# Kernel optimization log

Measured on AMD Instinct MI355X. Metric: run time of the kernel, lower is better.

Reference implementation:

```python
import jax, jax.numpy as jnp
import numpy as np

# ---- p4m group tables (g = 4*m + r, m in {0,1} mirror, r in {0..3} rot90) ----
def _p4m_tables():
    R = np.array([[0, -1], [1, 0]])
    F = np.array([[-1, 0], [0, 1]])
    I = np.eye(2, dtype=int)
    mats = []
    for m in (0, 1):
        for r in range(4):
            mats.append(np.linalg.matrix_power(R, r) @ (F if m else I))
    def idx(M):
        for i, A in enumerate(mats):
            if np.array_equal(A, M):
                return i
        raise ValueError('not in group')
    comp = np.array([[idx(mats[a] @ mats[b]) for b in range(8)] for a in range(8)])
    inv = np.array([idx(mats[a].T) for a in range(8)])  # orthogonal -> inv = transpose
    return comp, inv

COMP, INV = _p4m_tables()

def _transform_kernel(g, W):
    # L_g applied to filter spatial axes: mirror (last axis) then rotate r times
    m, r = g // 4, g % 4
    if m:
        W = jnp.flip(W, axis=-1)
    return jnp.rot90(W, k=r, axes=(-2, -1))

STRIDE, PADDING, DILATION = 1, 1, 1

def setup_inputs() -> dict:
    key = jax.random.key(0)
    k1, k2 = jax.random.split(key)
    B, Cin, Cout, H, W, kH, kW = 16, 64, 64, 64, 64, 3, 3
    x = jax.random.normal(k1, (B, Cin, 8, H, W), dtype=jnp.float32)
    scale = 1.0 / np.sqrt(Cin * kH * kW)
    weight_rel = jax.random.normal(k2, (Cout, Cin, 8, kH, kW), dtype=jnp.float32) * scale
    bias = jnp.zeros((Cout,), dtype=jnp.float32)
    return {'x': x, 'weight_rel': weight_rel, 'bias': bias}

def _gconv(x, weight_rel, bias):
    B, Cin, N, H, Wd = x.shape  # N == 8
    Cout, _, _, kH, kW = weight_rel.shape
    # Build the full group-equivariant filter bank once (fused form of the
    # original 64 small conv2d calls): bank[g*Cout+co, c*8+h] = L_g psi(g^{-1} h)
    banks = []
    for g in range(8):
        u = COMP[INV[g]]                # [8] relative element u = g^{-1} h, for h=0..7
        Wg = weight_rel[:, :, u]        # [Cout, Cin, 8, kH, kW]
        banks.append(_transform_kernel(g, Wg))
    bank = jnp.stack(banks, 0)          # [8, Cout, Cin, 8, kH, kW]
    bank = bank.reshape(8 * Cout, Cin * 8, kH, kW)
    x2 = x.reshape(B, Cin * 8, H, Wd)   # in-channel index = c*8 + h, matches bank
    y = jax.lax.conv_general_dilated(
        x2, bank,
        window_strides=(STRIDE, STRIDE),
        padding=[(PADDING, PADDING), (PADDING, PADDING)],
        rhs_dilation=(DILATION, DILATION),
        dimension_numbers=('NCHW', 'OIHW', 'NCHW'))
    Ho, Wo = y.shape[-2], y.shape[-1]
    y = y.reshape(B, 8, Cout, Ho, Wo).transpose(0, 2, 1, 3, 4)  # [B, Cout, 8, Ho, Wo]
    return y + bias[None, :, None, None, None]

def reference(x, weight_rel, bias):
    return _gconv(x, weight_rel, bias)
```

## Files before the change

### kernel.cpp

```cpp
#include <hip/hip_runtime.h>
#include <stdint.h>

typedef short  bf16x8 __attribute__((ext_vector_type(8)));
typedef float  f32x4  __attribute__((ext_vector_type(4)));


__device__ __forceinline__ short f2bf(float f) {
    uint32_t u = __builtin_bit_cast(uint32_t, f);
    u += 0x7FFFu + ((u >> 16) & 1u);
    return (short)(u >> 16);
}

__device__ __forceinline__ int u_index(int g, int s) {
    int r  = g & 3, m  = g >> 2;
    int r2 = s & 3, ms = s >> 2;
    if (!m) { int rr = (r2 - r) & 3; return ms ? (4 + rr) : rr; }
    else    { int rr = (r - r2) & 3; return ms ? rr : (4 + rr); }
}

__device__ __forceinline__ void gload_lds16(const void* g, void* l) {
    __builtin_amdgcn_global_load_lds(
        (const __attribute__((address_space(1))) uint32_t*)g,
        (__attribute__((address_space(3))) uint32_t*)l, 16, 0, 0);
}

#define XB_BYTES  (16LL * 66 * 66 * 512 * 2)
#define BK_BYTES  (16LL * 9 * 4 * 512 * 8 * 2)
#define WS_NEEDED (XB_BYTES + BK_BYTES)


__global__ __launch_bounds__(256) void prep_x2(const float* __restrict__ x,
                                               short* __restrict__ xb) {
    __shared__ float t[64][65];
    const int h = blockIdx.x, kc8 = blockIdx.y, b = blockIdx.z;
    const int k0 = kc8 * 64;
    const int tid = threadIdx.x;
    const int w  = tid & 63, kq = tid >> 6;
    const float* xp = x + ((size_t)(b * 512 + k0 + kq) * 4096) + h * 64 + w;
    #pragma unroll
    for (int i = 0; i < 16; ++i)
        t[kq + 4 * i][w] = xp[(size_t)(4 * i) * 4096];
    __syncthreads();
    const int w2 = tid >> 3, kk = tid & 7;
    #pragma unroll
    for (int half = 0; half < 2; ++half) {
        const int ww = w2 + 32 * half;
        bf16x8 v;
        #pragma unroll
        for (int j = 0; j < 8; ++j) v[j] = f2bf(t[kk * 8 + j][ww]);
        size_t o = (((size_t)b * 66 + h + 1) * 66 + (ww + 1)) * 512 + k0 + kk * 8;
        *reinterpret_cast<bf16x8*>(&xb[o]) = v;
    }
}

__global__ __launch_bounds__(256) void zero_border(short* __restrict__ xb) {
    int idx = blockIdx.x * 256 + threadIdx.x;
    if (idx >= 16 * 260 * 64) return;
    int kg = idx & 63;
    int rest = idx >> 6;
    int b  = rest / 260;
    int pe = rest - b * 260;
    int hh, ww;
    if      (pe < 66)  { hh = 0;            ww = pe; }
    else if (pe < 132) { hh = 65;           ww = pe - 66; }
    else if (pe < 196) { hh = pe - 132 + 1; ww = 0; }
    else               { hh = pe - 196 + 1; ww = 65; }
    size_t o = (((size_t)b * 66 + hh) * 66 + ww) * 512 + kg * 8;
    bf16x8 z = {0,0,0,0,0,0,0,0};
    *reinterpret_cast<bf16x8*>(&xb[o]) = z;
}

__global__ __launch_bounds__(256) void prep_w(const float* __restrict__ wrel,
                                              short* __restrict__ bank) {
    int tg = blockIdx.x * 256 + threadIdx.x;
    int oc = tg & 511;
    int kg = (tg >> 9) & 3;
    int kc = (tg >> 11) & 15;
    int t  = tg >> 15;
    int ki = t / 3, kj = t - ki * 3;
    int g = oc & 7, co = oc >> 3;
    int r = g & 3, m = g >> 2;
    int a0, b0;
    switch (r) {
        case 0:  a0 = ki;     b0 = kj;     break;
        case 1:  a0 = kj;     b0 = 2 - ki; break;
        case 2:  a0 = 2 - ki; b0 = 2 - kj; break;
        default: a0 = 2 - kj; b0 = ki;     break;
    }
    if (m) b0 = 2 - b0;
    int ci = kc * 4 + kg;
    const float* wp = wrel + (size_t)(co * 64 + ci) * 72 + a0 * 3 + b0;
    bf16x8 v;
    #pragma unroll
    for (int j = 0; j < 8; ++j) v[j] = f2bf(wp[u_index(g, j) * 9]);
    size_t o = ((((size_t)kc * 9 + t) * 4 + kg) * 512 + oc) * 8;
    *reinterpret_cast<bf16x8*>(&bank[o]) = v;
}

#define XS_SLOTS 39
#define XS_SH    (XS_SLOTS * 512)
#define WS_SH    (36 * 512)

#define STAGE(XS, WS, kc)                                                  \
    {                                                                      \
        _Pragma("unroll")                                                  \
        for (int q = 0; q < 9; ++q) {                                      \
            int it = wid + 4 * q;                                          \
            gload_lds16(bank + (size_t)(kc) * 147456 + woff[q],            \
                        &WS[it * 512]);                                    \
        }                                                                  \
        _Pragma("unroll")                                                  \
        for (int q = 0; q < 10; ++q) {                                     \
            int it = wid + 4 * q;                                          \
            if (it < XS_SLOTS)                                             \
                gload_lds16(xb + (size_t)xoff[q] + (kc) * 32,              \
                            &XS[it * 512]);                                \
        }                                                                  \
    }

#define COMPUTE(XS, WS)                                                    \
    {                                                                      \
        _Pragma("unroll")                                                  \
        for (int t = 0; t < 9; ++t) {                                      \
            const int ki = t / 3, kj = t - (t / 3) * 3;                    \
            bf16x8 a[4];                                                   \
            _Pragma("unroll")                                              \
            for (int mi = 0; mi < 4; ++mi)                                 \
                a[mi] = *reinterpret_cast<const bf16x8*>(                  \
                    &WS[((t * 4 + lkg) * 64 + mi * 16 + l15) * 8]);        \
            _Pragma("unroll")                                              \
            for (int nj = 0; nj < 8; ++nj) {                               \
                const int row = wid * 4 + (nj & 3) + ki;                   \
                const int col = (nj >> 2) * 16 + l15 + kj;                 \
                bf16x8 bv = *reinterpret_cast<const bf16x8*>(              \
                    &XS[(lkg * 624 + row * 34 + col) * 8]);                \
                _Pragma("unroll")                                          \
                for (int mi = 0; mi < 4; ++mi)                             \
                    acc[mi][nj] = __builtin_amdgcn_mfma_f32_16x16x32_bf16( \
                        a[mi], bv, acc[mi][nj], 0, 0, 0);                  \
            }                                                              \
        }                                                                  \
    }

__global__ __launch_bounds__(256, 1) void gconv_mfma(
    const short* __restrict__ xb, const short* __restrict__ bank,
    const float* __restrict__ bias, float* __restrict__ out)
{
    __shared__ __attribute__((aligned(16))) short xsA[XS_SH], xsB[XS_SH];
    __shared__ __attribute__((aligned(16))) short wsA[WS_SH], wsB[WS_SH];

    const int st  = blockIdx.x;
    const int ot  = blockIdx.y;
    const int b   = blockIdx.z;
    const int h0  = (st >> 1) * 16;
    const int w0  = (st & 1) * 32;
    const int oc0 = ot * 64;

    const int tid  = threadIdx.x;
    const int lane = tid & 63;
    const int wid  = tid >> 6;
    const int l15  = lane & 15;
    const int lkg  = lane >> 4;

    f32x4 acc[4][8];
    #pragma unroll
    for (int i = 0; i < 4; ++i)
        #pragma unroll
        for (int j = 0; j < 8; ++j)
            #pragma unroll
            for (int e = 0; e < 4; ++e) acc[i][j][e] = 0.f;

    const int xrow_base = (b * 66 + h0) * 66 + w0;

    int xoff[10];
    #pragma unroll
    for (int q = 0; q < 10; ++q) {
        int it = wid + 4 * q;
        if (it >= XS_SLOTS) it = XS_SLOTS - 1;
        int slot = it * 64 + lane;
        int kg = slot / 624;
        int px = slot - kg * 624;
        px = px < 612 ? px : 611;
        int r = px / 34;
        int c = px - r * 34;
        xoff[q] = (xrow_base + r * 66 + c) * 512 + kg * 8;
    }
    int woff[9];
    #pragma unroll
    for (int q = 0; q < 9; ++q) {
        int it = wid + 4 * q;
        int t  = it >> 2, kg = it & 3;
        woff[q] = ((t * 4 + kg) * 512 + oc0 + lane) * 8;
    }

    STAGE(xsA, wsA, 0);
    __syncthreads();
    for (int kc2 = 0; kc2 < 8; ++kc2) {
        STAGE(xsB, wsB, 2 * kc2 + 1);
        COMPUTE(xsA, wsA);
        __syncthreads();
        if (kc2 < 7) STAGE(xsA, wsA, 2 * kc2 + 2);
        COMPUTE(xsB, wsB);
        __syncthreads();
    }

    #pragma unroll
    for (int mi = 0; mi < 4; ++mi) {
        #pragma unroll
        for (int j = 0; j < 4; ++j) {
            const int oc_g = oc0 + mi * 16 + lkg * 4 + j;
            const float bv = bias[oc_g >> 3];
            float* op = out + ((size_t)b * 512 + oc_g) * 4096;
            #pragma unroll
            for (int nj = 0; nj < 8; ++nj) {
                const int hh = h0 + wid * 4 + (nj & 3);
                const int wwp = w0 + (nj >> 2) * 16 + l15;
                op[hh * 64 + wwp] = acc[mi][nj][j] + bv;
            }
        }
    }
}

__global__ __launch_bounds__(256) void gconv_direct(
    const float* __restrict__ x, const float* __restrict__ wrel,
    const float* __restrict__ bias, float* __restrict__ out)
{
    __shared__ float xsf[18][20];
    __shared__ float wsf[16][9];
    const int st = blockIdx.x, ct = blockIdx.y, b = blockIdx.z;
    const int h0 = (st >> 2) * 16, w0 = (st & 3) * 16, oc0 = ct * 16;
    const int tid = threadIdx.x;
    const int ch = tid & 15, blk = tid >> 4;
    const int by = (blk >> 2) * 4, bx = (blk & 3) * 4;
    const int oc = oc0 + ch, g = oc & 7, co = oc >> 3;
    const int wl_c = tid / 9, wl_k = tid - wl_c * 9;
    const int wl_i = wl_k / 3, wl_j = wl_k - wl_i * 3;
    const int wl_oc = oc0 + wl_c, wl_g = wl_oc & 7, wl_co = wl_oc >> 3;
    int a0, b0;
    { const int r = wl_g & 3, m = wl_g >> 2;
      switch (r) { case 0: a0=wl_i; b0=wl_j; break; case 1: a0=wl_j; b0=2-wl_i; break;
                   case 2: a0=2-wl_i; b0=2-wl_j; break; default: a0=2-wl_j; b0=wl_i; break; }
      if (m) b0 = 2 - b0; }
    float acc[4][4];
    #pragma unroll
    for (int i=0;i<4;++i) for (int j=0;j<4;++j) acc[i][j]=0.f;
    for (int t = 0; t < 512; ++t) {
        const int ci = t >> 3, s = t & 7;
        __syncthreads();
        const float* xp = x + (((size_t)(b * 64 + ci) * 8 + s) * 4096);
        for (int idx = tid; idx < 18 * 18; idx += 256) {
            const int rr = idx / 18, cc = idx - rr * 18;
            const int gh = h0 - 1 + rr, gw = w0 - 1 + cc;
            float v = 0.f;
            if (gh >= 0 && gh < 64 && gw >= 0 && gw < 64) v = xp[gh * 64 + gw];
            xsf[rr][cc] = v;
        }
        if (tid < 144) {
            const int u = u_index(wl_g, s);
            wsf[wl_c][wl_k] = wrel[((size_t)(wl_co*64+ci)*8+u)*9 + a0*3 + b0];
        }
        __syncthreads();
        float wr[9];
        #pragma unroll
        for (int k=0;k<9;++k) wr[k]=wsf[ch][k];
        float xv[6][6];
        #pragma unroll
        for (int i=0;i<6;++i) for (int j=0;j<6;++j) xv[i][j]=xsf[by+i][bx+j];
        #pragma unroll
        for (int py=0;py<4;++py) for (int px=0;px<4;++px)
            for (int ki=0;ki<3;++ki) for (int kj=0;kj<3;++kj)
                acc[py][px] += xv[py+ki][px+kj]*wr[ki*3+kj];
    }
    const float bv = bias[co];
    float* op = out + (((size_t)(b*64+co)*8+g)*4096);
    #pragma unroll
    for (int py=0;py<4;++py) for (int px=0;px<4;++px)
        op[(h0+by+py)*64 + (w0+bx+px)] = acc[py][px] + bv;
}

extern "C" void kernel_launch(void* const* d_in, const int* in_sizes, int n_in,
                              void* d_out, int out_size, void* d_ws, size_t ws_size,
                              hipStream_t stream) {
    const float* x    = (const float*)d_in[0];
    const float* wrel = (const float*)d_in[1];
    const float* bias = (const float*)d_in[2];
    float* out        = (float*)d_out;

    if (ws_size >= (size_t)WS_NEEDED) {
        short* xb   = (short*)d_ws;
        short* bank = (short*)((char*)d_ws + XB_BYTES);
        zero_border<<<1040, 256, 0, stream>>>(xb);
        {
            dim3 g(64, 8, 16);
            prep_x2<<<g, 256, 0, stream>>>(x, xb);
        }
        prep_w<<<1152, 256, 0, stream>>>(wrel, bank);
        dim3 grid(8, 8, 16);
        gconv_mfma<<<grid, 256, 0, stream>>>(xb, bank, bias, out);
    } else {
        dim3 grid(16, 32, 16);
        gconv_direct<<<grid, 256, 0, stream>>>(x, wrel, bias, out);
    }
}
```

Before: 327.5 us.

## Shrink MFMA tile to 16x16 pixels, pipeline weights per kernel column, reuse B fragments

The implicit-GEMM conv kernel's spatial tile shrinks from 16x32 to 16x16 pixels, doubling the grid. Weights are now staged per kernel column (kj), using a reordered bank layout and smaller double buffers. Each column's six input-row fragments are loaded once into registers and reused across the three ki taps. The much smaller LDS and accumulator footprint allows two blocks per CU for more latency hiding. The cost is more syncs per K chunk and more halo reloads per output, since the smaller tile overlaps its neighbours more.

```diff
diff --git a/kernel.cpp b/kernel.cpp
--- a/kernel.cpp
+++ b/kernel.cpp
@@ -93,47 +93,52 @@
     bf16x8 v;
     #pragma unroll
     for (int j = 0; j < 8; ++j) v[j] = f2bf(wp[u_index(g, j) * 9]);
-    size_t o = ((((size_t)kc * 9 + t) * 4 + kg) * 512 + oc) * 8;
+    size_t o = (((((size_t)kc * 3 + kj) * 3 + ki) * 4 + kg) * 512 + oc) * 8;
     *reinterpret_cast<bf16x8*>(&bank[o]) = v;
 }
 
-#define XS_SLOTS 39
-#define XS_SH    (XS_SLOTS * 512)
-#define WS_SH    (36 * 512)
-
-#define STAGE(XS, WS, kc)                                                  \
+#define XS_SH (1344 * 8)
+#define WB_SH (768 * 8)
+
+#define STAGE_X(XS, kc)                                                    \
     {                                                                      \
         _Pragma("unroll")                                                  \
-        for (int q = 0; q < 9; ++q) {                                      \
+        for (int q = 0; q < 6; ++q) {                                      \
             int it = wid + 4 * q;                                          \
-            gload_lds16(bank + (size_t)(kc) * 147456 + woff[q],            \
-                        &WS[it * 512]);                                    \
-        }                                                                  \
-        _Pragma("unroll")                                                  \
-        for (int q = 0; q < 10; ++q) {                                     \
-            int it = wid + 4 * q;                                          \
-            if (it < XS_SLOTS)                                             \
+            if (it < 21)                                                   \
                 gload_lds16(xb + (size_t)xoff[q] + (kc) * 32,              \
                             &XS[it * 512]);                                \
         }                                                                  \
     }
 
-#define COMPUTE(XS, WS)                                                    \
+#define STAGE_W(WB, kc, kj)                                                \
     {                                                                      \
         _Pragma("unroll")                                                  \
-        for (int t = 0; t < 9; ++t) {                                      \
-            const int ki = t / 3, kj = t - (t / 3) * 3;                    \
+        for (int q = 0; q < 3; ++q) {                                      \
+            int it = wid + 4 * q;                                          \
+            gload_lds16(bank + (size_t)((kc) * 3 + (kj)) * 49152           \
+                             + woff[q],                                    \
+                        &WB[it * 512]);                                    \
+        }                                                                  \
+    }
+
+#define COMPUTE_KJ(XS, WB, kj)                                             \
+    {                                                                      \
+        bf16x8 bfr[6];                                                     \
+        _Pragma("unroll")                                                  \
+        for (int rr = 0; rr < 6; ++rr)                                     \
+            bfr[rr] = *reinterpret_cast<const bf16x8*>(                    \
+                &XS[(lkg * 336 + (wid * 4 + rr) * 18 + l15 + (kj)) * 8]);  \
+        _Pragma("unroll")                                                  \
+        for (int ki = 0; ki < 3; ++ki) {                                   \
             bf16x8 a[4];                                                   \
             _Pragma("unroll")                                              \
             for (int mi = 0; mi < 4; ++mi)                                 \
                 a[mi] = *reinterpret_cast<const bf16x8*>(                  \
-                    &WS[((t * 4 + lkg) * 64 + mi * 16 + l15) * 8]);        \
+                    &WB[((ki * 4 + lkg) * 64 + mi * 16 + l15) * 8]);       \
             _Pragma("unroll")                                              \
-            for (int nj = 0; nj < 8; ++nj) {                               \
-                const int row = wid * 4 + (nj & 3) + ki;                   \
-                const int col = (nj >> 2) * 16 + l15 + kj;                 \
-                bf16x8 bv = *reinterpret_cast<const bf16x8*>(              \
-                    &XS[(lkg * 624 + row * 34 + col) * 8]);                \
+            for (int nj = 0; nj < 4; ++nj) {                               \
+                bf16x8 bv = bfr[nj + ki];                                  \
                 _Pragma("unroll")                                          \
                 for (int mi = 0; mi < 4; ++mi)                             \
                     acc[mi][nj] = __builtin_amdgcn_mfma_f32_16x16x32_bf16( \
@@ -142,18 +147,32 @@
         }                                                                  \
     }
 
-__global__ __launch_bounds__(256, 1) void gconv_mfma(
+#define CHUNK(kc, XC, XN, W0, W1)                                          \
+    {                                                                      \
+        STAGE_W(W1, kc, 1);                                                \
+        COMPUTE_KJ(XC, W0, 0);                                             \
+        __syncthreads();                                                   \
+        STAGE_W(W0, kc, 2);                                                \
+        if ((kc) < 15) STAGE_X(XN, (kc) + 1);                              \
+        COMPUTE_KJ(XC, W1, 1);                                             \
+        __syncthreads();                                                   \
+        if ((kc) < 15) STAGE_W(W1, (kc) + 1, 0);                           \
+        COMPUTE_KJ(XC, W0, 2);                                             \
+        __syncthreads();                                                   \
+    }
+
+__global__ __launch_bounds__(256, 2) void gconv_mfma(
     const short* __restrict__ xb, const short* __restrict__ bank,
     const float* __restrict__ bias, float* __restrict__ out)
 {
     __shared__ __attribute__((aligned(16))) short xsA[XS_SH], xsB[XS_SH];
-    __shared__ __attribute__((aligned(16))) short wsA[WS_SH], wsB[WS_SH];
+    __shared__ __attribute__((aligned(16))) short wbA[WB_SH], wbB[WB_SH];
 
     const int st  = blockIdx.x;
     const int ot  = blockIdx.y;
     const int b   = blockIdx.z;
-    const int h0  = (st >> 1) * 16;
-    const int w0  = (st & 1) * 32;
+    const int h0  = (st >> 2) * 16;
+    const int w0  = (st & 3) * 16;
     const int oc0 = ot * 64;
 
     const int tid  = threadIdx.x;
@@ -162,46 +181,42 @@
     const int l15  = lane & 15;
     const int lkg  = lane >> 4;
 
-    f32x4 acc[4][8];
+    f32x4 acc[4][4];
     #pragma unroll
     for (int i = 0; i < 4; ++i)
         #pragma unroll
-        for (int j = 0; j < 8; ++j)
+        for (int j = 0; j < 4; ++j)
             #pragma unroll
             for (int e = 0; e < 4; ++e) acc[i][j][e] = 0.f;
 
     const int xrow_base = (b * 66 + h0) * 66 + w0;
 
-    int xoff[10];
-    #pragma unroll
-    for (int q = 0; q < 10; ++q) {
+    int xoff[6];
+    #pragma unroll
+    for (int q = 0; q < 6; ++q) {
         int it = wid + 4 * q;
-        if (it >= XS_SLOTS) it = XS_SLOTS - 1;
+        if (it > 20) it = 20;
         int slot = it * 64 + lane;
-        int kg = slot / 624;
-        int px = slot - kg * 624;
-        px = px < 612 ? px : 611;
-        int r = px / 34;
-        int c = px - r * 34;
+        int kg = slot / 336;
+        int px = slot - kg * 336;
+        px = px < 324 ? px : 323;
+        int r = px / 18;
+        int c = px - r * 18;
         xoff[q] = (xrow_base + r * 66 + c) * 512 + kg * 8;
     }
-    int woff[9];
-    #pragma unroll
-    for (int q = 0; q < 9; ++q) {
+    int woff[3];
+    #pragma unroll
+    for (int q = 0; q < 3; ++q) {
         int it = wid + 4 * q;
-        int t  = it >> 2, kg = it & 3;
-        woff[q] = ((t * 4 + kg) * 512 + oc0 + lane) * 8;
-    }
-
-    STAGE(xsA, wsA, 0);
+        woff[q] = (it * 512 + oc0 + lane) * 8;
+    }
+
+    STAGE_X(xsA, 0);
+    STAGE_W(wbA, 0, 0);
     __syncthreads();
     for (int kc2 = 0; kc2 < 8; ++kc2) {
-        STAGE(xsB, wsB, 2 * kc2 + 1);
-        COMPUTE(xsA, wsA);
-        __syncthreads();
-        if (kc2 < 7) STAGE(xsA, wsA, 2 * kc2 + 2);
-        COMPUTE(xsB, wsB);
-        __syncthreads();
+        CHUNK(2 * kc2,     xsA, xsB, wbA, wbB);
+        CHUNK(2 * kc2 + 1, xsB, xsA, wbB, wbA);
     }
 
     #pragma unroll
@@ -212,10 +227,9 @@
             const float bv = bias[oc_g >> 3];
             float* op = out + ((size_t)b * 512 + oc_g) * 4096;
             #pragma unroll
-            for (int nj = 0; nj < 8; ++nj) {
-                const int hh = h0 + wid * 4 + (nj & 3);
-                const int wwp = w0 + (nj >> 2) * 16 + l15;
-                op[hh * 64 + wwp] = acc[mi][nj][j] + bv;
+            for (int nj = 0; nj < 4; ++nj) {
+                const int hh = h0 + wid * 4 + nj;
+                op[hh * 64 + w0 + l15] = acc[mi][nj][j] + bv;
             }
         }
     }
@@ -295,7 +309,7 @@
             prep_x2<<<g, 256, 0, stream>>>(x, xb);
         }
         prep_w<<<1152, 256, 0, stream>>>(wrel, bank);
-        dim3 grid(8, 8, 16);
+        dim3 grid(16, 8, 16);
         gconv_mfma<<<grid, 256, 0, stream>>>(xb, bank, bias, out);
     } else {
         dim3 grid(16, 32, 16);
```

Measured after the change: 301.7 us. 7.9% less time.

## Cache input fragments in registers across kernel rows and triple-buffer weights per column

Applied to the files above, without the earlier changes.

The filter bank is reordered so each kernel column (kj) forms its own contiguous weight slab. The main loop keeps a single input tile in LDS. For each kj it loads six input rows of B fragments into registers once and reuses them across the three kernel rows, instead of re-reading LDS for every tap. Weights are streamed through three small LDS buffers, with MFMA priority raised via setprio. LDS use is low enough for launch bounds to allow two blocks per CU; in exchange there are more barriers per channel chunk and more register pressure.

```diff
diff --git a/kernel.cpp b/kernel.cpp
--- a/kernel.cpp
+++ b/kernel.cpp
@@ -93,61 +93,75 @@
     bf16x8 v;
     #pragma unroll
     for (int j = 0; j < 8; ++j) v[j] = f2bf(wp[u_index(g, j) * 9]);
-    size_t o = ((((size_t)kc * 9 + t) * 4 + kg) * 512 + oc) * 8;
+    size_t o = (((((size_t)kc * 3 + kj) * 3 + ki) * 4 + kg) * 512 + oc) * 8;
     *reinterpret_cast<bf16x8*>(&bank[o]) = v;
 }
 
-#define XS_SLOTS 39
-#define XS_SH    (XS_SLOTS * 512)
-#define WS_SH    (36 * 512)
-
-#define STAGE(XS, WS, kc)                                                  \
+#define XS_SH (39 * 512)
+#define WB_SH (12 * 512)
+
+#define STAGE_X(kc)                                                        \
     {                                                                      \
-        _Pragma("unroll")                                                  \
-        for (int q = 0; q < 9; ++q) {                                      \
-            int it = wid + 4 * q;                                          \
-            gload_lds16(bank + (size_t)(kc) * 147456 + woff[q],            \
-                        &WS[it * 512]);                                    \
-        }                                                                  \
         _Pragma("unroll")                                                  \
         for (int q = 0; q < 10; ++q) {                                     \
             int it = wid + 4 * q;                                          \
-            if (it < XS_SLOTS)                                             \
+            if (it < 39)                                                   \
                 gload_lds16(xb + (size_t)xoff[q] + (kc) * 32,              \
-                            &XS[it * 512]);                                \
+                            &xs[it * 512]);                                \
         }                                                                  \
     }
 
-#define COMPUTE(XS, WS)                                                    \
+#define STAGE_W(WB, kc, kj)                                                \
     {                                                                      \
         _Pragma("unroll")                                                  \
-        for (int t = 0; t < 9; ++t) {                                      \
-            const int ki = t / 3, kj = t - (t / 3) * 3;                    \
+        for (int q = 0; q < 3; ++q) {                                      \
+            int it = wid + 4 * q;                                          \
+            gload_lds16(bank + (size_t)((kc) * 3 + (kj)) * 49152           \
+                             + woff[q],                                    \
+                        &WB[it * 512]);                                    \
+        }                                                                  \
+    }
+
+#define READ_B(DST, kj)                                                    \
+    {                                                                      \
+        _Pragma("unroll")                                                  \
+        for (int rr = 0; rr < 6; ++rr)                                     \
+            _Pragma("unroll")                                              \
+            for (int cg = 0; cg < 2; ++cg)                                 \
+                DST[rr][cg] = *reinterpret_cast<const bf16x8*>(            \
+                    &xs[(lkg * 624 + (wid * 4 + rr) * 34 + cg * 16         \
+                         + l15 + (kj)) * 8]);                              \
+    }
+
+#define MFMA_KJ(BS, WB)                                                    \
+    {                                                                      \
+        _Pragma("unroll")                                                  \
+        for (int ki = 0; ki < 3; ++ki) {                                   \
             bf16x8 a[4];                                                   \
             _Pragma("unroll")                                              \
             for (int mi = 0; mi < 4; ++mi)                                 \
                 a[mi] = *reinterpret_cast<const bf16x8*>(                  \
-                    &WS[((t * 4 + lkg) * 64 + mi * 16 + l15) * 8]);        \
+                    &WB[((ki * 4 + lkg) * 64 + mi * 16 + l15) * 8]);       \
+            __builtin_amdgcn_s_setprio(1);                                 \
             _Pragma("unroll")                                              \
             for (int nj = 0; nj < 8; ++nj) {                               \
-                const int row = wid * 4 + (nj & 3) + ki;                   \
-                const int col = (nj >> 2) * 16 + l15 + kj;                 \
-                bf16x8 bv = *reinterpret_cast<const bf16x8*>(              \
-                    &XS[(lkg * 624 + row * 34 + col) * 8]);                \
+                bf16x8 bv = BS[(nj & 3) + ki][nj >> 2];                    \
                 _Pragma("unroll")                                          \
                 for (int mi = 0; mi < 4; ++mi)                             \
                     acc[mi][nj] = __builtin_amdgcn_mfma_f32_16x16x32_bf16( \
                         a[mi], bv, acc[mi][nj], 0, 0, 0);                  \
             }                                                              \
+            __builtin_amdgcn_s_setprio(0);                                 \
         }                                                                  \
     }
 
-__global__ __launch_bounds__(256, 1) void gconv_mfma(
+__global__ __launch_bounds__(256, 2) void gconv_mfma(
     const short* __restrict__ xb, const short* __restrict__ bank,
     const float* __restrict__ bias, float* __restrict__ out)
 {
-    __shared__ __attribute__((aligned(16))) short xsA[XS_SH], xsB[XS_SH];
-    __shared__ __attribute__((aligned(16))) short wsA[WS_SH], wsB[WS_SH];
+    __shared__ __attribute__((aligned(16))) short xs[XS_SH];
+    __shared__ __attribute__((aligned(16))) short wb0[WB_SH], wb1[WB_SH],
+                                                  wb2[WB_SH];
 
     const int st  = blockIdx.x;
     const int ot  = blockIdx.y;
@@ -176,7 +190,7 @@
     #pragma unroll
     for (int q = 0; q < 10; ++q) {
         int it = wid + 4 * q;
-        if (it >= XS_SLOTS) it = XS_SLOTS - 1;
+        if (it > 38) it = 38;
         int slot = it * 64 + lane;
         int kg = slot / 624;
         int px = slot - kg * 624;
@@ -185,22 +199,34 @@
         int c = px - r * 34;
         xoff[q] = (xrow_base + r * 66 + c) * 512 + kg * 8;
     }
-    int woff[9];
-    #pragma unroll
-    for (int q = 0; q < 9; ++q) {
+    int woff[3];
+    #pragma unroll
+    for (int q = 0; q < 3; ++q) {
         int it = wid + 4 * q;
-        int t  = it >> 2, kg = it & 3;
-        woff[q] = ((t * 4 + kg) * 512 + oc0 + lane) * 8;
-    }
-
-    STAGE(xsA, wsA, 0);
+        woff[q] = (it * 512 + oc0 + lane) * 8;
+    }
+
+    bf16x8 bP[6][2], bQ[6][2];
+
+    STAGE_X(0);
+    STAGE_W(wb0, 0, 0);
+    STAGE_W(wb1, 0, 1);
     __syncthreads();
-    for (int kc2 = 0; kc2 < 8; ++kc2) {
-        STAGE(xsB, wsB, 2 * kc2 + 1);
-        COMPUTE(xsA, wsA);
-        __syncthreads();
-        if (kc2 < 7) STAGE(xsA, wsA, 2 * kc2 + 2);
-        COMPUTE(xsB, wsB);
+
+    for (int kc = 0; kc < 16; ++kc) {
+        const int kcn = kc < 15 ? kc + 1 : 15;
+        READ_B(bP, 0);
+        STAGE_W(wb2, kc, 2);
+        READ_B(bQ, 1);
+        MFMA_KJ(bP, wb0);
+        __syncthreads();
+        STAGE_W(wb0, kcn, 0);
+        READ_B(bP, 2);
+        MFMA_KJ(bQ, wb1);
+        __syncthreads();
+        STAGE_W(wb1, kcn, 1);
+        STAGE_X(kcn);
+        MFMA_KJ(bP, wb2);
         __syncthreads();
     }
 
```

Result: slower. 473.6 us (+44.6%).
